# Performance work log

Measured on AMD Instinct MI355X. Metric: run time of the kernel, lower is better.

## Reference

```python
import jax, jax.numpy as jnp
import numpy as np

NBINS_PIX = 256   # uint8 pixel values
NBINS_MEAN = 512  # neighbor mean fits in [0, 408] for side=1


def setup_inputs() -> dict:
    key = jax.random.key(0)
    # uniform [0,1) so x.max() < 1.0 branch (x*255 quantization) is taken, as in the source
    x = jax.random.uniform(key, (64, 1024, 1024), dtype=jnp.float32)
    return {"x": x}


def reference(x):
    H, W = x.shape[-2:]
    x = jax.lax.stop_gradient(x)  # mirrors .clone().detach()
    xf = x.reshape(-1, H, W)
    B = xf.shape[0]
    # quantize: (x*255).to(uint8) if max<1 else x.to(uint8); uint8 cast truncates
    scale = jnp.where(jnp.max(xf) < 1.0, jnp.float32(255.0), jnp.float32(1.0))
    xq = (xf * scale).astype(jnp.uint8).astype(jnp.float32)
    xi = xq.astype(jnp.int32)

    # zero-padded 8-neighbor sum (3x3 window minus center), side=1
    xp = jnp.pad(xi, ((0, 0), (1, 1), (1, 1)))
    nb = jnp.zeros_like(xi)
    for dh in range(3):
        for dw in range(3):
            if dh == 1 and dw == 1:
                continue
            nb = nb + xp[:, dh:dh + H, dw:dw + W]

    # Faithful replication of the source's normalization: the original indexes
    # mean_nb[a, b] where dim0 is the BATCH dim and dim1 is the row dim, so the
    # divisor depends on (batch, row) and broadcasts over columns.
    # t=0: num=3 at 4 (batch,row) corners; then num->5 for edges and interior.
    D = jnp.ones((B, H), dtype=jnp.float32)
    D = D.at[0, 0].set(3.0).at[-1, 0].set(3.0).at[0, -1].set(3.0).at[-1, -1].set(3.0)
    D = D.at[1:-1, 0].set(5.0).at[1:-1, -1].set(5.0)
    D = D.at[0, 1:-1].set(5.0).at[-1, 1:-1].set(5.0)
    D = D.at[1:-1, 1:-1].set(5.0)
    mean_nb = nb.astype(jnp.float32) / D[:, :, None]
    mean_i = mean_nb.astype(jnp.int32)  # trunc toward zero, values >= 0

    # joint (pixel, mean) histogram per image -> entropy, matches unique+counts
    codes = xi * NBINS_MEAN + mean_i  # in [0, 256*512)

    def hist_entropy(c):
        counts = jnp.zeros(NBINS_PIX * NBINS_MEAN, jnp.float32).at[c.reshape(-1)].add(1.0)
        p = counts / (H * W)
        safe = jnp.where(p > 0, p, 1.0)
        return jnp.sum(jnp.where(p > 0, -p * jnp.log2(safe), 0.0))

    ent = jax.vmap(hist_entropy)(codes)  # [B]
    return jnp.mean(ent)
```

## Files before the change

### kernel.cpp

```cpp
#include <hip/hip_runtime.h>

#define IMG_H 1024
#define IMG_W 1024
#define NPIX  (IMG_H * IMG_W)
#define NBINS (256 * 512)
#define TILE  64
#define LW    (TILE + 2)

#define MEANS  428
#define HBINS  (256 * MEANS)
#define HWORDS (HBINS / 4)
#define QUADS  4
#define QROWS  (IMG_H / QUADS)
#define TCOLS  8
#define TROWS  (QROWS / 8)

__global__ __launch_bounds__(1024) void fused_hist_kernel(const float* __restrict__ x,
                                                          unsigned int* __restrict__ partials,
                                                          int B) {
    __shared__ unsigned int h[HWORDS];

    const int blk  = blockIdx.x;
    const int b    = blk >> 2;
    const int quad = blk & 3;
    const int tid  = threadIdx.x;

    for (int i = tid; i < HWORDS; i += 1024) h[i] = 0u;
    __syncthreads();

    const float* img = x + (size_t)b * NPIX;
    const int c0    = (tid & 127) * TCOLS;
    const int strip = tid >> 7;
    const int rs    = quad * QROWS + strip * TROWS;
    const int re    = rs + TROWS;
    const bool bEdge = (b == 0) || (b == B - 1);

    auto loadraw = [&](int r, float4& f0, float4& f1, float& fl, float& fr) {
        if ((unsigned)r < IMG_H) {
            const float* row = img + r * IMG_W;
            f0 = *(const float4*)(row + c0);
            f1 = *(const float4*)(row + c0 + 4);
            fl = (c0 > 0) ? row[c0 - 1] : 0.0f;
            fr = (c0 + TCOLS < IMG_W) ? row[c0 + TCOLS] : 0.0f;
        } else {
            f0 = make_float4(0.f, 0.f, 0.f, 0.f);
            f1 = make_float4(0.f, 0.f, 0.f, 0.f);
            fl = 0.f; fr = 0.f;
        }
    };
    auto hsumq = [&](const float4& f0, const float4& f1, float fl, float fr,
                     int hs[TCOLS], int qc[TCOLS]) {
        int q[10];
        q[0] = (int)(fl   * 255.0f);
        q[1] = (int)(f0.x * 255.0f);
        q[2] = (int)(f0.y * 255.0f);
        q[3] = (int)(f0.z * 255.0f);
        q[4] = (int)(f0.w * 255.0f);
        q[5] = (int)(f1.x * 255.0f);
        q[6] = (int)(f1.y * 255.0f);
        q[7] = (int)(f1.z * 255.0f);
        q[8] = (int)(f1.w * 255.0f);
        q[9] = (int)(fr   * 255.0f);
#pragma unroll
        for (int i = 0; i < TCOLS; ++i) { hs[i] = q[i] + q[i + 1] + q[i + 2]; qc[i] = q[i + 1]; }
    };

    int hA[TCOLS], hB[TCOLS], qB[TCOLS];
    {
        float4 f0, f1; float fl, fr; int qt[TCOLS];
        loadraw(rs - 1, f0, f1, fl, fr); hsumq(f0, f1, fl, fr, hA, qt);
    }
    {
        float4 f0, f1; float fl, fr;
        loadraw(rs, f0, f1, fl, fr); hsumq(f0, f1, fl, fr, hB, qB);
    }
    float4 n0a, n0b, n1a, n1b; float n0l, n0r, n1l, n1r;
    loadraw(rs + 1, n0a, n0b, n0l, n0r);
    loadraw(rs + 2, n1a, n1b, n1l, n1r);

    for (int r = rs; r < re; r += 2) {
        float4 u0a = n0a, u0b = n0b, u1a = n1a, u1b = n1b;
        float  u0l = n0l, u0r = n0r, u1l = n1l, u1r = n1r;
        loadraw(r + 3, n0a, n0b, n0l, n0r);
        loadraw(r + 4, n1a, n1b, n1l, n1r);

        int hC[TCOLS], qC[TCOLS], hD[TCOLS], qD[TCOLS];
        hsumq(u0a, u0b, u0l, u0r, hC, qC);
        hsumq(u1a, u1b, u1l, u1r, hD, qD);

        const bool c0n = bEdge && (r == 0);
        const bool c1n = bEdge && (r + 1 == IMG_H - 1);

#pragma unroll
        for (int i = 0; i < TCOLS; ++i) {
            int nb = hA[i] + hB[i] + hC[i] - qB[i];
            unsigned mean = c0n ? (unsigned)nb / 3u : (unsigned)nb / 5u;
            unsigned bin  = (unsigned)qB[i] * MEANS + mean;
            atomicAdd(&h[bin >> 2], 1u << ((bin & 3u) * 8u));
        }
#pragma unroll
        for (int i = 0; i < TCOLS; ++i) {
            int nb = hB[i] + hC[i] + hD[i] - qC[i];
            unsigned mean = c1n ? (unsigned)nb / 3u : (unsigned)nb / 5u;
            unsigned bin  = (unsigned)qC[i] * MEANS + mean;
            atomicAdd(&h[bin >> 2], 1u << ((bin & 3u) * 8u));
        }
#pragma unroll
        for (int i = 0; i < TCOLS; ++i) { hA[i] = hC[i]; hB[i] = hD[i]; qB[i] = qD[i]; }
    }
    __syncthreads();

    unsigned int* dst = partials + (size_t)blk * HWORDS;
    for (int i = tid; i < HWORDS; i += 1024) dst[i] = h[i];
}

__global__ __launch_bounds__(256) void merge_entropy_kernel(const unsigned int* __restrict__ partials,
                                                            double* __restrict__ acc,
                                                            int B) {
    const int w   = blockIdx.x * 256 + threadIdx.x;
    const int img = blockIdx.y;
    const unsigned int* p = partials + (size_t)img * QUADS * HWORDS + w;
    unsigned w0 = p[0], w1 = p[HWORDS], w2 = p[2 * HWORDS], w3 = p[3 * HWORDS];

    double local = 0.0;
#pragma unroll
    for (int sh = 0; sh < 32; sh += 8) {
        unsigned c = ((w0 >> sh) & 255u) + ((w1 >> sh) & 255u)
                   + ((w2 >> sh) & 255u) + ((w3 >> sh) & 255u);
        if (c) local += (double)c * (20.0 - (double)log2f((float)c));
    }
    for (int off = 32; off > 0; off >>= 1)
        local += __shfl_down(local, off, 64);

    __shared__ double sacc[4];
    const int lane = threadIdx.x & 63;
    const int wid  = threadIdx.x >> 6;
    if (lane == 0) sacc[wid] = local;
    __syncthreads();
    if (threadIdx.x == 0)
        atomicAdd(acc, sacc[0] + sacc[1] + sacc[2] + sacc[3]);
}

__global__ void finalize_kernel(const double* __restrict__ acc,
                                float* __restrict__ out, int B) {
    out[0] = (float)(acc[0] / ((double)NPIX * (double)B));
}

__global__ __launch_bounds__(256) void hist_kernel(const float* __restrict__ x,
                                                   unsigned int* __restrict__ hist,
                                                   int B) {
    __shared__ int s[LW * LW];
    const int tilesPerRow = IMG_W / TILE;
    const int tilesPerImg = (IMG_H / TILE) * tilesPerRow;
    const int b   = blockIdx.x / tilesPerImg;
    const int t   = blockIdx.x % tilesPerImg;
    const int ty0 = (t / tilesPerRow) * TILE;
    const int tx0 = (t % tilesPerRow) * TILE;
    const float* img = x + (size_t)b * NPIX;
    const int tid = threadIdx.x;

    for (int i = tid; i < LW * LW; i += 256) {
        int r = i / LW, c = i - r * LW;
        int gy = ty0 + r - 1, gx = tx0 + c - 1;
        int v = 0;
        if ((unsigned)gy < IMG_H && (unsigned)gx < IMG_W)
            v = (int)(img[gy * IMG_W + gx] * 255.0f);
        s[i] = v;
    }
    __syncthreads();

    unsigned int* hb = hist + (size_t)b * NBINS;
    const bool bEdge = (b == 0) || (b == B - 1);
    const int tx = tid & 63, sy = tid >> 6;
    const int c = tx + 1, r0 = sy * 16;

    int h0, h1, m1;
    { int a = s[r0 * LW + c - 1], m = s[r0 * LW + c], d = s[r0 * LW + c + 1]; h0 = a + m + d; }
    { int a = s[(r0 + 1) * LW + c - 1], m = s[(r0 + 1) * LW + c], d = s[(r0 + 1) * LW + c + 1]; h1 = a + m + d; m1 = m; }

    for (int ry = r0; ry < r0 + 16; ++ry) {
        int a = s[(ry + 2) * LW + c - 1], m = s[(ry + 2) * LW + c], d = s[(ry + 2) * LW + c + 1];
        int h2 = a + m + d;
        int nb = h0 + h1 + h2 - m1;
        int gy = ty0 + ry;
        unsigned mean = (unsigned)nb / 5u;
        if (bEdge && (gy == 0 || gy == IMG_H - 1)) mean = (unsigned)nb / 3u;
        atomicAdd(&hb[m1 * 512 + (int)mean], 1u);
        h0 = h1; h1 = h2; m1 = m;
    }
}

__global__ __launch_bounds__(256) void entropy_kernel(const unsigned int* __restrict__ hist,
                                                      double* __restrict__ acc, int n) {
    double local = 0.0;
    const int stride = gridDim.x * 256;
    for (int i = blockIdx.x * 256 + threadIdx.x; i < n; i += stride) {
        unsigned int cv = hist[i];
        if (cv) local += (double)cv * (20.0 - (double)log2f((float)cv));
    }
    for (int off = 32; off > 0; off >>= 1)
        local += __shfl_down(local, off, 64);
    __shared__ double sacc[4];
    const int lane = threadIdx.x & 63, wid = threadIdx.x >> 6;
    if (lane == 0) sacc[wid] = local;
    __syncthreads();
    if (threadIdx.x == 0)
        atomicAdd(acc, sacc[0] + sacc[1] + sacc[2] + sacc[3]);
}

extern "C" void kernel_launch(void* const* d_in, const int* in_sizes, int n_in,
                              void* d_out, int out_size, void* d_ws, size_t ws_size,
                              hipStream_t stream) {
    const float* x = (const float*)d_in[0];
    const int B = in_sizes[0] / NPIX;

    const size_t partBytes = (size_t)B * QUADS * HWORDS * sizeof(unsigned int);

    if (ws_size >= partBytes + 64) {
        unsigned int* partials = (unsigned int*)d_ws;
        double* acc = (double*)((char*)d_ws + partBytes);
        hipMemsetAsync(acc, 0, sizeof(double), stream);

        fused_hist_kernel<<<B * QUADS, 1024, 0, stream>>>(x, partials, B);
        merge_entropy_kernel<<<dim3(HWORDS / 256, B), 256, 0, stream>>>(partials, acc, B);
        finalize_kernel<<<1, 1, 0, stream>>>(acc, (float*)d_out, B);
    } else {
        unsigned int* hist = (unsigned int*)d_ws;
        const size_t histBytes = (size_t)B * NBINS * sizeof(unsigned int);
        double* acc = (double*)((char*)d_ws + histBytes);
        hipMemsetAsync(d_ws, 0, histBytes + sizeof(double), stream);

        const int tilesPerImg = (IMG_H / TILE) * (IMG_W / TILE);
        hist_kernel<<<B * tilesPerImg, 256, 0, stream>>>(x, hist, B);
        entropy_kernel<<<1024, 256, 0, stream>>>(hist, acc, B * NBINS);
        finalize_kernel<<<1, 1, 0, stream>>>(acc, (float*)d_out, B);
    }
}
```

Measured before the change: 452.7 us.

## Pack column sums into 16-bit lanes, deepen row prefetch, overlap loads with zeroing

```diff
diff --git a/kernel.cpp b/kernel.cpp
--- a/kernel.cpp
+++ b/kernel.cpp
@@ -10,6 +10,7 @@
 #define MEANS  428
 #define HBINS  (256 * MEANS)
 #define HWORDS (HBINS / 4)
+#define HVECS  (HWORDS / 4)
 #define QUADS  4
 #define QROWS  (IMG_H / QUADS)
 #define TCOLS  8
@@ -18,15 +19,12 @@
 __global__ __launch_bounds__(1024) void fused_hist_kernel(const float* __restrict__ x,
                                                           unsigned int* __restrict__ partials,
                                                           int B) {
-    __shared__ unsigned int h[HWORDS];
+    __shared__ __align__(16) unsigned int h[HWORDS];
 
     const int blk  = blockIdx.x;
     const int b    = blk >> 2;
     const int quad = blk & 3;
     const int tid  = threadIdx.x;
-
-    for (int i = tid; i < HWORDS; i += 1024) h[i] = 0u;
-    __syncthreads();
 
     const float* img = x + (size_t)b * NPIX;
     const int c0    = (tid & 127) * TCOLS;
@@ -48,70 +46,99 @@
             fl = 0.f; fr = 0.f;
         }
     };
-    auto hsumq = [&](const float4& f0, const float4& f1, float fl, float fr,
-                     int hs[TCOLS], int qc[TCOLS]) {
-        int q[10];
-        q[0] = (int)(fl   * 255.0f);
-        q[1] = (int)(f0.x * 255.0f);
-        q[2] = (int)(f0.y * 255.0f);
-        q[3] = (int)(f0.z * 255.0f);
-        q[4] = (int)(f0.w * 255.0f);
-        q[5] = (int)(f1.x * 255.0f);
-        q[6] = (int)(f1.y * 255.0f);
-        q[7] = (int)(f1.z * 255.0f);
-        q[8] = (int)(f1.w * 255.0f);
-        q[9] = (int)(fr   * 255.0f);
-#pragma unroll
-        for (int i = 0; i < TCOLS; ++i) { hs[i] = q[i] + q[i + 1] + q[i + 2]; qc[i] = q[i + 1]; }
-    };
-
-    int hA[TCOLS], hB[TCOLS], qB[TCOLS];
-    {
-        float4 f0, f1; float fl, fr; int qt[TCOLS];
-        loadraw(rs - 1, f0, f1, fl, fr); hsumq(f0, f1, fl, fr, hA, qt);
-    }
-    {
-        float4 f0, f1; float fl, fr;
-        loadraw(rs, f0, f1, fl, fr); hsumq(f0, f1, fl, fr, hB, qB);
-    }
-    float4 n0a, n0b, n1a, n1b; float n0l, n0r, n1l, n1r;
+
+    auto hsump = [&](const float4& f0, const float4& f1, float fl, float fr,
+                     unsigned hs[4], unsigned qc[4]) {
+        unsigned q0 = (unsigned)(int)(fl   * 255.0f);
+        unsigned q1 = (unsigned)(int)(f0.x * 255.0f);
+        unsigned q2 = (unsigned)(int)(f0.y * 255.0f);
+        unsigned q3 = (unsigned)(int)(f0.z * 255.0f);
+        unsigned q4 = (unsigned)(int)(f0.w * 255.0f);
+        unsigned q5 = (unsigned)(int)(f1.x * 255.0f);
+        unsigned q6 = (unsigned)(int)(f1.y * 255.0f);
+        unsigned q7 = (unsigned)(int)(f1.z * 255.0f);
+        unsigned q8 = (unsigned)(int)(f1.w * 255.0f);
+        unsigned q9 = (unsigned)(int)(fr   * 255.0f);
+        unsigned p0 = q0 | (q1 << 16);
+        unsigned p1 = q2 | (q3 << 16);
+        unsigned p2 = q4 | (q5 << 16);
+        unsigned p3 = q6 | (q7 << 16);
+        unsigned p4 = q8 | (q9 << 16);
+        unsigned m0 = (p0 >> 16) | (p1 << 16);
+        unsigned m1 = (p1 >> 16) | (p2 << 16);
+        unsigned m2 = (p2 >> 16) | (p3 << 16);
+        unsigned m3 = (p3 >> 16) | (p4 << 16);
+        hs[0] = p0 + m0 + p1;  qc[0] = m0;
+        hs[1] = p1 + m1 + p2;  qc[1] = m1;
+        hs[2] = p2 + m2 + p3;  qc[2] = m2;
+        hs[3] = p3 + m3 + p4;  qc[3] = m3;
+    };
+
+    unsigned hA[4], hB[4], qB[4];
+
+    auto emit = [&](const unsigned hU[4], const unsigned hM[4], const unsigned qM[4],
+                    const unsigned hL[4], bool div3) {
+#pragma unroll
+        for (int j = 0; j < 4; ++j) {
+            unsigned nb = hU[j] + hM[j] + hL[j] - qM[j];
+            unsigned n0 = nb & 0xFFFFu, n1 = nb >> 16;
+            unsigned cv0 = qM[j] & 0xFFFFu, cv1 = qM[j] >> 16;
+            unsigned me0 = div3 ? n0 / 3u : n0 / 5u;
+            unsigned me1 = div3 ? n1 / 3u : n1 / 5u;
+            unsigned bin0 = cv0 * MEANS + me0;
+            unsigned bin1 = cv1 * MEANS + me1;
+            atomicAdd(&h[bin0 >> 2], 1u << ((bin0 & 3u) * 8u));
+            atomicAdd(&h[bin1 >> 2], 1u << ((bin1 & 3u) * 8u));
+        }
+    };
+
+    auto body = [&](int r, float4& a0, float4& a1, float& al, float& ar,
+                          float4& b0, float4& b1, float& bl, float& br) {
+        unsigned hC[4], qC[4], hD[4], qD[4];
+        hsump(a0, a1, al, ar, hC, qC);
+        hsump(b0, b1, bl, br, hD, qD);
+        if (r + 5 <= re) loadraw(r + 5, a0, a1, al, ar);
+        if (r + 6 <= re) loadraw(r + 6, b0, b1, bl, br);
+        const bool c0n = bEdge && (r == 0);
+        const bool c1n = bEdge && (r + 1 == IMG_H - 1);
+        emit(hA, hB, qB, hC, c0n);
+        emit(hB, hC, qC, hD, c1n);
+#pragma unroll
+        for (int j = 0; j < 4; ++j) { hA[j] = hC[j]; hB[j] = hD[j]; qB[j] = qD[j]; }
+    };
+
+    float4 e0a, e0b, e1a, e1b;  float e0l, e0r, e1l, e1r;
+    float4 n0a, n0b, n1a, n1b, n2a, n2b, n3a, n3b;
+    float  n0l, n0r, n1l, n1r, n2l, n2r, n3l, n3r;
+    loadraw(rs - 1, e0a, e0b, e0l, e0r);
+    loadraw(rs,     e1a, e1b, e1l, e1r);
     loadraw(rs + 1, n0a, n0b, n0l, n0r);
     loadraw(rs + 2, n1a, n1b, n1l, n1r);
-
-    for (int r = rs; r < re; r += 2) {
-        float4 u0a = n0a, u0b = n0b, u1a = n1a, u1b = n1b;
-        float  u0l = n0l, u0r = n0r, u1l = n1l, u1r = n1r;
-        loadraw(r + 3, n0a, n0b, n0l, n0r);
-        loadraw(r + 4, n1a, n1b, n1l, n1r);
-
-        int hC[TCOLS], qC[TCOLS], hD[TCOLS], qD[TCOLS];
-        hsumq(u0a, u0b, u0l, u0r, hC, qC);
-        hsumq(u1a, u1b, u1l, u1r, hD, qD);
-
-        const bool c0n = bEdge && (r == 0);
-        const bool c1n = bEdge && (r + 1 == IMG_H - 1);
-
-#pragma unroll
-        for (int i = 0; i < TCOLS; ++i) {
-            int nb = hA[i] + hB[i] + hC[i] - qB[i];
-            unsigned mean = c0n ? (unsigned)nb / 3u : (unsigned)nb / 5u;
-            unsigned bin  = (unsigned)qB[i] * MEANS + mean;
-            atomicAdd(&h[bin >> 2], 1u << ((bin & 3u) * 8u));
+    loadraw(rs + 3, n2a, n2b, n2l, n2r);
+    loadraw(rs + 4, n3a, n3b, n3l, n3r);
+
+    {
+        uint4* h4 = (uint4*)h;
+#pragma unroll
+        for (int i = 0; i < 7; ++i) {
+            int idx = tid + i * 1024;
+            if (idx < HVECS) h4[idx] = make_uint4(0u, 0u, 0u, 0u);
         }
-#pragma unroll
-        for (int i = 0; i < TCOLS; ++i) {
-            int nb = hB[i] + hC[i] + hD[i] - qC[i];
-            unsigned mean = c1n ? (unsigned)nb / 3u : (unsigned)nb / 5u;
-            unsigned bin  = (unsigned)qC[i] * MEANS + mean;
-            atomicAdd(&h[bin >> 2], 1u << ((bin & 3u) * 8u));
-        }
-#pragma unroll
-        for (int i = 0; i < TCOLS; ++i) { hA[i] = hC[i]; hB[i] = hD[i]; qB[i] = qD[i]; }
-    }
-    __syncthreads();
-
-    unsigned int* dst = partials + (size_t)blk * HWORDS;
-    for (int i = tid; i < HWORDS; i += 1024) dst[i] = h[i];
+    }
+    __syncthreads();
+
+    { unsigned tq[4]; hsump(e0a, e0b, e0l, e0r, hA, tq); }
+    hsump(e1a, e1b, e1l, e1r, hB, qB);
+
+    for (int r = rs; r < re; r += 4) {
+        body(r,     n0a, n0b, n0l, n0r, n1a, n1b, n1l, n1r);
+        body(r + 2, n2a, n2b, n2l, n2r, n3a, n3b, n3l, n3r);
+    }
+    __syncthreads();
+
+    uint4* dst4 = (uint4*)(partials + (size_t)blk * HWORDS);
+    const uint4* s4 = (const uint4*)h;
+    for (int i = tid; i < HVECS; i += 1024) dst4[i] = s4[i];
 }
 
 __global__ __launch_bounds__(256) void merge_entropy_kernel(const unsigned int* __restrict__ partials,
```

Result: no change. 455.5 us (median of 2 runs) (+0.6%).
